# Kernel optimization log

Measured on AMD Instinct MI355X. Metric: run time of the kernel, lower is better.

Reference implementation:

```python
import jax, jax.numpy as jnp
import numpy as np

INPUT_SIZE = 512
OUTPUT_CLASS = 2
BATCH, INST_NUM = 4, 40000


def setup_inputs() -> dict:
    key = jax.random.key(0)
    ks = jax.random.split(key, 8)
    s_in = 1.0 / np.sqrt(INPUT_SIZE)
    s_h = 1.0 / np.sqrt(128)
    return {
        "feats": jax.random.normal(ks[0], (BATCH, INST_NUM, INPUT_SIZE), jnp.float32),
        "c": jax.random.normal(ks[1], (BATCH, INST_NUM, OUTPUT_CLASS), jnp.float32),
        "q_w1": jax.random.uniform(ks[2], (INPUT_SIZE, 128), jnp.float32, -s_in, s_in),
        "q_b1": jax.random.uniform(ks[3], (128,), jnp.float32, -s_in, s_in),
        "q_w2": jax.random.uniform(ks[4], (128, 128), jnp.float32, -s_h, s_h),
        "q_b2": jax.random.uniform(ks[5], (128,), jnp.float32, -s_h, s_h),
        "fcc_w": jax.random.uniform(ks[6], (OUTPUT_CLASS, OUTPUT_CLASS, INPUT_SIZE), jnp.float32, -s_in, s_in),
        "fcc_b": jax.random.uniform(ks[7], (OUTPUT_CLASS,), jnp.float32, -s_in, s_in),
    }


def _q_mlp(x, w1, b1, w2, b2):
    h = jax.nn.relu(x @ w1 + b1)
    return jnp.tanh(h @ w2 + b2)


def reference(feats, c, q_w1, q_b1, q_w2, q_b2, fcc_w, fcc_b):
    batch, inst_num, dim = feats.shape
    V = feats  # passing_v=False -> Identity
    Q = _q_mlp(feats, q_w1, q_b1, q_w2, q_b2)  # [b, n, 128]
    # top instance per class: sort descending, take first -> argmax along instances
    top_idx = jnp.argmax(c, axis=1)  # [b, output_class]
    m_feats = jnp.take_along_axis(feats, top_idx[:, :, None], axis=1)  # [b, oc, dim]
    q_max = _q_mlp(m_feats, q_w1, q_b1, q_w2, q_b2)  # [b, oc, 128]
    # NOTE: original divides by sqrt(Q.shape[1]) == sqrt(inst_num)
    scale = jnp.sqrt(jnp.float32(inst_num))
    A = jnp.einsum('bnk,bok->bno', Q, q_max) / scale  # [b, n, oc]
    A = jax.nn.softmax(A, axis=1)  # softmax over instances
    B = jnp.einsum('bno,bnd->bod', A, V)  # [b, oc, dim]
    # Conv1d(oc, oc, kernel=dim) on B -> full contraction over (in_ch, dim)
    C = jnp.einsum('bid,oid->bo', B, fcc_w) + fcc_b  # [b, oc]
    return C, A, B
```

## Files before the change

kernel.cpp:

```cpp
#include <hip/hip_runtime.h>
#include <hip/hip_bf16.h>

#define NB 4
#define NI 40000
#define DI 512
#define NH 128
#define TM 32
#define NT 1250

typedef __attribute__((ext_vector_type(8))) short bf16x8;
typedef __attribute__((ext_vector_type(4))) float f32x4;

__device__ __forceinline__ ushort f2b(float f) {
    union { float f; unsigned u; } x; x.f = f;
    unsigned r = x.u + 0x7FFFu + ((x.u >> 16) & 1u);
    return (ushort)(r >> 16);
}
__device__ __forceinline__ float b2f(ushort u) {
    union { unsigned u; float f; } x; x.u = ((unsigned)u) << 16;
    return x.f;
}

__global__ void k_wt(const float* __restrict__ w1, const float* __restrict__ w2,
                     ushort* __restrict__ w1t, ushort* __restrict__ w2t) {
    int idx = blockIdx.x * 256 + threadIdx.x;
    if (idx < 65536) {
        int j = idx >> 9, i = idx & 511;
        w1t[idx] = f2b(w1[i * 128 + j]);
    } else if (idx < 81920) {
        int r = idx - 65536;
        int j = r >> 7, k = r & 127;
        w2t[r] = f2b(w2[k * 128 + j]);
    }
}

__global__ void k_am1(const float* __restrict__ c, float* __restrict__ pv, int* __restrict__ pi) {
    int blk = blockIdx.x;
    int bo = blk >> 4, ch = blk & 15;
    int b = bo >> 1, o = bo & 1;
    __shared__ float rv[256];
    __shared__ int   ri[256];
    int tid = threadIdx.x;
    float bv = -3.402823466e38f; int bi = 0x7fffffff;
    for (int n = ch * 2500 + tid; n < (ch + 1) * 2500; n += 256) {
        float v = c[((size_t)b * NI + n) * 2 + o];
        if (v > bv || (v == bv && n < bi)) { bv = v; bi = n; }
    }
    rv[tid] = bv; ri[tid] = bi;
    __syncthreads();
    for (int s = 128; s > 0; s >>= 1) {
        if (tid < s) {
            if (rv[tid + s] > rv[tid] || (rv[tid + s] == rv[tid] && ri[tid + s] < ri[tid])) {
                rv[tid] = rv[tid + s]; ri[tid] = ri[tid + s];
            }
        }
        __syncthreads();
    }
    if (tid == 0) { pv[blk] = rv[0]; pi[blk] = ri[0]; }
}

__global__ void k_am2(const float* __restrict__ pv, const int* __restrict__ pi,
                      int* __restrict__ topidx) {
    int bo = blockIdx.x;
    if (threadIdx.x == 0) {
        float bv = -3.402823466e38f; int bi = 0x7fffffff;
        for (int ch = 0; ch < 16; ++ch) {
            float v = pv[bo * 16 + ch]; int idx = pi[bo * 16 + ch];
            if (v > bv || (v == bv && idx < bi)) { bv = v; bi = idx; }
        }
        topidx[bo] = bi;
    }
}

__global__ void k_qmax(const float* __restrict__ feats, const int* __restrict__ topidx,
                       const float* __restrict__ w1, const float* __restrict__ b1,
                       const float* __restrict__ w2, const float* __restrict__ b2,
                       float* __restrict__ qmax) {
    int bo = blockIdx.x;
    int b = bo >> 1;
    __shared__ float xs[DI];
    __shared__ float hs[NH];
    int tid = threadIdx.x;
    const float* x = feats + ((size_t)b * NI + topidx[bo]) * DI;
    if (tid < DI) xs[tid] = x[tid];
    __syncthreads();
    int j = tid >> 2, part = tid & 3;
    float p = 0.f;
    for (int i = part * 128; i < part * 128 + 128; ++i)
        p += xs[i] * w1[i * NH + j];
    p += __shfl_xor(p, 1); p += __shfl_xor(p, 2);
    if (part == 0) { float h = p + b1[j]; hs[j] = h > 0.f ? h : 0.f; }
    __syncthreads();
    p = 0.f;
    for (int i = part * 32; i < part * 32 + 32; ++i)
        p += hs[i] * w2[i * NH + j];
    p += __shfl_xor(p, 1); p += __shfl_xor(p, 2);
    if (part == 0) qmax[bo * NH + j] = tanhf(p + b2[j]);
}

__global__ __launch_bounds__(256, 3)
void k_main(const float* __restrict__ feats,
            const ushort* __restrict__ w1t, const ushort* __restrict__ w2t,
            const float* __restrict__ b1, const float* __restrict__ b2,
            const float* __restrict__ qmax,
            float* __restrict__ s_ws, float* __restrict__ zp, float* __restrict__ Up) {
    __shared__ ushort x_lds[TM * 512];
    __shared__ ushort h_lds[TM * 128];
    __shared__ float  sp_lds[4][TM][2];
    __shared__ float  e_lds[TM * 2];
    __shared__ float  qm_lds[2 * NH];

    const int tid = threadIdx.x;
    const int b = blockIdx.x / NT;
    const int t = blockIdx.x % NT;
    const int n0 = t * TM;

    qm_lds[tid] = qmax[b * 256 + tid];

    const float4* xg4 = (const float4*)(feats + ((size_t)(b * NI + n0)) * DI);
#pragma unroll
    for (int q = 0; q < 16; ++q) {
        int idx = tid + q * 256;
        int row = idx >> 7;
        int c4  = idx & 127;
        float4 v = xg4[idx];
        ushort4 u;
        u.x = f2b(v.x); u.y = f2b(v.y); u.z = f2b(v.z); u.w = f2b(v.w);
        int byteoff = (c4 * 8) ^ ((row & 7) << 4);
        *(ushort4*)((char*)x_lds + row * 1024 + byteoff) = u;
    }
    __syncthreads();

    const int wn = tid >> 6;
    const int lane = tid & 63;
    const int lr = lane & 15;
    const int lk = (lane >> 4) * 8;
    const int l4 = (lane >> 4) * 4;
    const int xsw = (lr & 7) << 4;

    const char* xrow0 = (const char*)x_lds + lr * 1024;
    const char* xrow1 = (const char*)x_lds + (16 + lr) * 1024;
    const ushort* w1b0 = w1t + (size_t)(wn * 32 + lr) * DI + lk;
    const ushort* w1b1 = w1t + (size_t)(wn * 32 + 16 + lr) * DI + lk;

    f32x4 acc[2][2] = {};
#pragma unroll 4
    for (int ks = 0; ks < 16; ++ks) {
        int kb = (ks * 32 + lk) * 2;
        bf16x8 a0 = *(const bf16x8*)(xrow0 + (kb ^ xsw));
        bf16x8 a1 = *(const bf16x8*)(xrow1 + (kb ^ xsw));
        bf16x8 b0 = *(const bf16x8*)(w1b0 + ks * 32);
        bf16x8 b1v = *(const bf16x8*)(w1b1 + ks * 32);
        acc[0][0] = __builtin_amdgcn_mfma_f32_16x16x32_bf16(a0, b0,  acc[0][0], 0, 0, 0);
        acc[0][1] = __builtin_amdgcn_mfma_f32_16x16x32_bf16(a0, b1v, acc[0][1], 0, 0, 0);
        acc[1][0] = __builtin_amdgcn_mfma_f32_16x16x32_bf16(a1, b0,  acc[1][0], 0, 0, 0);
        acc[1][1] = __builtin_amdgcn_mfma_f32_16x16x32_bf16(a1, b1v, acc[1][1], 0, 0, 0);
    }

#pragma unroll
    for (int m = 0; m < 2; ++m)
#pragma unroll
        for (int n = 0; n < 2; ++n) {
            int col = wn * 32 + n * 16 + lr;
            float bias = b1[col];
#pragma unroll
            for (int r = 0; r < 4; ++r) {
                int row = m * 16 + l4 + r;
                float v = acc[m][n][r] + bias;
                *(ushort*)((char*)h_lds + row * 256 + ((col * 2) ^ ((row & 7) << 4))) =
                    f2b(v > 0.f ? v : 0.f);
            }
        }
    __syncthreads();

    f32x4 acc2[2][2] = {};
#pragma unroll
    for (int ks = 0; ks < 4; ++ks) {
        int kb = (ks * 32 + lk) * 2;
        bf16x8 a0 = *(const bf16x8*)((const char*)h_lds + lr * 256 + (kb ^ xsw));
        bf16x8 a1 = *(const bf16x8*)((const char*)h_lds + (16 + lr) * 256 + (kb ^ xsw));
        bf16x8 b0 = *(const bf16x8*)(w2t + (wn * 32 + lr) * NH + ks * 32 + lk);
        bf16x8 b1v = *(const bf16x8*)(w2t + (wn * 32 + 16 + lr) * NH + ks * 32 + lk);
        acc2[0][0] = __builtin_amdgcn_mfma_f32_16x16x32_bf16(a0, b0,  acc2[0][0], 0, 0, 0);
        acc2[0][1] = __builtin_amdgcn_mfma_f32_16x16x32_bf16(a0, b1v, acc2[0][1], 0, 0, 0);
        acc2[1][0] = __builtin_amdgcn_mfma_f32_16x16x32_bf16(a1, b0,  acc2[1][0], 0, 0, 0);
        acc2[1][1] = __builtin_amdgcn_mfma_f32_16x16x32_bf16(a1, b1v, acc2[1][1], 0, 0, 0);
    }

#pragma unroll
    for (int m = 0; m < 2; ++m)
#pragma unroll
        for (int r = 0; r < 4; ++r) {
            float p0 = 0.f, p1 = 0.f;
#pragma unroll
            for (int n = 0; n < 2; ++n) {
                int col = wn * 32 + n * 16 + lr;
                float q = tanhf(acc2[m][n][r] + b2[col]);
                p0 += q * qm_lds[col];
                p1 += q * qm_lds[NH + col];
            }
            p0 += __shfl_xor(p0, 1); p1 += __shfl_xor(p1, 1);
            p0 += __shfl_xor(p0, 2); p1 += __shfl_xor(p1, 2);
            p0 += __shfl_xor(p0, 4); p1 += __shfl_xor(p1, 4);
            p0 += __shfl_xor(p0, 8); p1 += __shfl_xor(p1, 8);
            if (lr == 0) {
                int row = m * 16 + l4 + r;
                sp_lds[wn][row][0] = p0;
                sp_lds[wn][row][1] = p1;
            }
        }
    __syncthreads();

    if (tid < 64) {
        int row = tid >> 1, o = tid & 1;
        float s = (sp_lds[0][row][o] + sp_lds[1][row][o] +
                   sp_lds[2][row][o] + sp_lds[3][row][o]) * 0.005f;
        s_ws[((size_t)(b * NI + n0 + row)) * 2 + o] = s;
        float e = expf(s);
        e_lds[row * 2 + o] = e;
        float z = e;
        z += __shfl_xor(z, 2);  z += __shfl_xor(z, 4);
        z += __shfl_xor(z, 8);  z += __shfl_xor(z, 16);
        z += __shfl_xor(z, 32);
        if (tid < 2) zp[(b * NT + t) * 2 + tid] = z;
    }
    __syncthreads();

    {
        int bc = tid * 4;
        float u00 = 0.f, u01 = 0.f, u10 = 0.f, u11 = 0.f;
#pragma unroll 8
        for (int n = 0; n < TM; ++n) {
            unsigned v = *(const unsigned*)((const char*)x_lds + n * 1024 + (bc ^ ((n & 7) << 4)));
            float x0 = b2f((ushort)(v & 0xffff));
            float x1 = b2f((ushort)(v >> 16));
            float e0 = e_lds[n * 2], e1 = e_lds[n * 2 + 1];
            u00 += e0 * x0; u01 += e0 * x1;
            u10 += e1 * x0; u11 += e1 * x1;
        }
        size_t base = ((size_t)(b * NT + t) * 2) * DI;
        float2 v0; v0.x = u00; v0.y = u01;
        float2 v1; v1.x = u10; v1.y = u11;
        *(float2*)&Up[base + tid * 2] = v0;
        *(float2*)&Up[base + DI + tid * 2] = v1;
    }
}

__global__ void k_zred(const float* __restrict__ zp, float* __restrict__ Zt) {
    int bo = blockIdx.x; int b = bo >> 1, o = bo & 1;
    __shared__ float red[256];
    int tid = threadIdx.x;
    float z = 0.f;
    for (int t = tid; t < NT; t += 256) z += zp[(b * NT + t) * 2 + o];
    red[tid] = z; __syncthreads();
    for (int s = 128; s > 0; s >>= 1) {
        if (tid < s) red[tid] += red[tid + s];
        __syncthreads();
    }
    if (tid == 0) Zt[bo] = red[0];
}

__global__ void k_A(const float* __restrict__ s_ws, const float* __restrict__ Zt,
                    float* __restrict__ outA) {
    int idx = blockIdx.x * 256 + threadIdx.x;
    int b = idx / (NI * 2);
    int o = idx & 1;
    outA[idx] = expf(s_ws[idx]) / Zt[b * 2 + o];
}

__global__ void k_B1(const float* __restrict__ Up, float* __restrict__ Up2) {
    int blk = blockIdx.x;
    int bo = blk / 25, cch = blk % 25;
    int b = bo >> 1, o = bo & 1;
    int d = threadIdx.x;
    float u = 0.f;
    for (int t = cch * 50; t < cch * 50 + 50; ++t)
        u += Up[(((size_t)(b * NT + t)) * 2 + o) * DI + d];
    Up2[(size_t)blk * DI + d] = u;
}

__global__ void k_B2(const float* __restrict__ Up2, const float* __restrict__ Zt,
                     float* __restrict__ outB) {
    int bo = blockIdx.x; int d = threadIdx.x;
    float u = 0.f;
    for (int cc = 0; cc < 25; ++cc) u += Up2[(size_t)(bo * 25 + cc) * DI + d];
    outB[bo * DI + d] = u / Zt[bo];
}

__global__ void k_C(const float* __restrict__ outB, const float* __restrict__ fcc_w,
                    const float* __restrict__ fcc_b, float* __restrict__ outC) {
    int bo = blockIdx.x; int b = bo >> 1, o = bo & 1;
    __shared__ float red[256];
    int tid = threadIdx.x;
    float acc = 0.f;
    for (int idx = tid; idx < 2 * DI; idx += 256) {
        int i = idx >> 9, d = idx & 511;
        acc += outB[(b * 2 + i) * DI + d] * fcc_w[o * (2 * DI) + i * DI + d];
    }
    red[tid] = acc; __syncthreads();
    for (int s = 128; s > 0; s >>= 1) {
        if (tid < s) red[tid] += red[tid + s];
        __syncthreads();
    }
    if (tid == 0) outC[bo] = red[0] + fcc_b[o];
}

extern "C" void kernel_launch(void* const* d_in, const int* in_sizes, int n_in,
                              void* d_out, int out_size, void* d_ws, size_t ws_size,
                              hipStream_t stream) {
    const float* feats = (const float*)d_in[0];
    const float* c     = (const float*)d_in[1];
    const float* q_w1  = (const float*)d_in[2];
    const float* q_b1  = (const float*)d_in[3];
    const float* q_w2  = (const float*)d_in[4];
    const float* q_b2  = (const float*)d_in[5];
    const float* fcc_w = (const float*)d_in[6];
    const float* fcc_b = (const float*)d_in[7];
    float* out = (float*)d_out;

    char* w = (char*)d_ws;
    ushort* w1t  = (ushort*)(w);
    ushort* w2t  = (ushort*)(w + 131072);
    float* qmaxb = (float*)(w + 163840);
    int*   topi  = (int*)(w + 167936);
    float* Zt    = (float*)(w + 167968);
    float* pv    = (float*)(w + 168000);
    int*   pi    = (int*)(w + 168512);
    float* s_ws  = (float*)(w + 169024);
    float* zp    = (float*)(w + 1449024);
    float* Up2   = (float*)(w + 1489024);
    float* Up    = (float*)(w + 1898624);

    float* outC = out;
    float* outA = out + 8;
    float* outB = out + 8 + NB * NI * 2;

    k_wt<<<320, 256, 0, stream>>>(q_w1, q_w2, w1t, w2t);
    k_am1<<<128, 256, 0, stream>>>(c, pv, pi);
    k_am2<<<8, 64, 0, stream>>>(pv, pi, topi);
    k_qmax<<<8, 512, 0, stream>>>(feats, topi, q_w1, q_b1, q_w2, q_b2, qmaxb);
    k_main<<<NB * NT, 256, 0, stream>>>(feats, w1t, w2t, q_b1, q_b2, qmaxb, s_ws, zp, Up);
    k_zred<<<8, 256, 0, stream>>>(zp, Zt);
    k_A<<<NB * NI * 2 / 256, 256, 0, stream>>>(s_ws, Zt, outA);
    k_B1<<<200, 512, 0, stream>>>(Up, Up2);
    k_B2<<<8, 512, 0, stream>>>(Up2, Zt, outB);
    k_C<<<8, 256, 0, stream>>>(outB, fcc_w, fcc_b, outC);
}
```

Baseline: 204.4 us.

## Restructure main kernel to per-wave 16-row tiles with direct global loads

The main kernel now gives each wave 16 rows of instances and all 128 hidden columns, reading feats straight from global into MFMA operands and dropping the shared x tile and most block barriers. It also stores exp scores so k_A skips the exp, swaps tanhf for a fast exp-based tanh, folds the argmax final step into k_qmax, and merges the two B reduction kernels into one. The aim is less LDS traffic, fewer syncs and fewer launches. In exchange feats is read twice from global (MLP and weighted sum), each lane loads the full w1 and w2 from global, and unnormalised exps are stored without max subtraction.

```diff
diff --git a/kernel.cpp b/kernel.cpp
--- a/kernel.cpp
+++ b/kernel.cpp
@@ -5,8 +5,6 @@
 #define NI 40000
 #define DI 512
 #define NH 128
-#define TM 32
-#define NT 1250
 
 typedef __attribute__((ext_vector_type(8))) short bf16x8;
 typedef __attribute__((ext_vector_type(4))) float f32x4;
@@ -16,9 +14,10 @@
     unsigned r = x.u + 0x7FFFu + ((x.u >> 16) & 1u);
     return (ushort)(r >> 16);
 }
-__device__ __forceinline__ float b2f(ushort u) {
-    union { unsigned u; float f; } x; x.u = ((unsigned)u) << 16;
-    return x.f;
+__device__ __forceinline__ float tanh_fast(float x) {
+    x = fminf(15.f, fmaxf(-15.f, x));
+    float e = __expf(2.f * x);
+    return (e - 1.f) / (e + 1.f);
 }
 
 __global__ void k_wt(const float* __restrict__ w1, const float* __restrict__ w2,
@@ -59,20 +58,8 @@
     if (tid == 0) { pv[blk] = rv[0]; pi[blk] = ri[0]; }
 }
 
-__global__ void k_am2(const float* __restrict__ pv, const int* __restrict__ pi,
-                      int* __restrict__ topidx) {
-    int bo = blockIdx.x;
-    if (threadIdx.x == 0) {
-        float bv = -3.402823466e38f; int bi = 0x7fffffff;
-        for (int ch = 0; ch < 16; ++ch) {
-            float v = pv[bo * 16 + ch]; int idx = pi[bo * 16 + ch];
-            if (v > bv || (v == bv && idx < bi)) { bv = v; bi = idx; }
-        }
-        topidx[bo] = bi;
-    }
-}
-
-__global__ void k_qmax(const float* __restrict__ feats, const int* __restrict__ topidx,
+__global__ void k_qmax(const float* __restrict__ feats,
+                       const float* __restrict__ pv, const int* __restrict__ pi,
                        const float* __restrict__ w1, const float* __restrict__ b1,
                        const float* __restrict__ w2, const float* __restrict__ b2,
                        float* __restrict__ qmax) {
@@ -80,8 +67,18 @@
     int b = bo >> 1;
     __shared__ float xs[DI];
     __shared__ float hs[NH];
+    __shared__ int s_idx;
     int tid = threadIdx.x;
-    const float* x = feats + ((size_t)b * NI + topidx[bo]) * DI;
+    if (tid == 0) {
+        float bv = -3.402823466e38f; int bi = 0x7fffffff;
+        for (int ch = 0; ch < 16; ++ch) {
+            float v = pv[bo * 16 + ch]; int idx = pi[bo * 16 + ch];
+            if (v > bv || (v == bv && idx < bi)) { bv = v; bi = idx; }
+        }
+        s_idx = bi;
+    }
+    __syncthreads();
+    const float* x = feats + ((size_t)b * NI + s_idx) * DI;
     if (tid < DI) xs[tid] = x[tid];
     __syncthreads();
     int j = tid >> 2, part = tid & 3;
@@ -99,150 +96,159 @@
 }
 
 __global__ __launch_bounds__(256, 3)
-void k_main(const float* __restrict__ feats,
-            const ushort* __restrict__ w1t, const ushort* __restrict__ w2t,
-            const float* __restrict__ b1, const float* __restrict__ b2,
-            const float* __restrict__ qmax,
-            float* __restrict__ s_ws, float* __restrict__ zp, float* __restrict__ Up) {
-    __shared__ ushort x_lds[TM * 512];
-    __shared__ ushort h_lds[TM * 128];
-    __shared__ float  sp_lds[4][TM][2];
-    __shared__ float  e_lds[TM * 2];
-    __shared__ float  qm_lds[2 * NH];
-
-    const int tid = threadIdx.x;
-    const int b = blockIdx.x / NT;
-    const int t = blockIdx.x % NT;
-    const int n0 = t * TM;
-
-    qm_lds[tid] = qmax[b * 256 + tid];
-
-    const float4* xg4 = (const float4*)(feats + ((size_t)(b * NI + n0)) * DI);
-#pragma unroll
-    for (int q = 0; q < 16; ++q) {
-        int idx = tid + q * 256;
-        int row = idx >> 7;
-        int c4  = idx & 127;
-        float4 v = xg4[idx];
-        ushort4 u;
-        u.x = f2b(v.x); u.y = f2b(v.y); u.z = f2b(v.z); u.w = f2b(v.w);
-        int byteoff = (c4 * 8) ^ ((row & 7) << 4);
-        *(ushort4*)((char*)x_lds + row * 1024 + byteoff) = u;
-    }
-    __syncthreads();
-
-    const int wn = tid >> 6;
+void k_mlp(const float* __restrict__ feats,
+           const ushort* __restrict__ w1t, const ushort* __restrict__ w2t,
+           const float* __restrict__ b1, const float* __restrict__ b2,
+           const float* __restrict__ qmax,
+           float* __restrict__ ews, float* __restrict__ zp, float* __restrict__ Up) {
+    __shared__ ushort h_lds[4][2048];
+    __shared__ float  u_lds[4][2][DI];
+
+    const int tid  = threadIdx.x;
+    const int wv   = tid >> 6;
     const int lane = tid & 63;
-    const int lr = lane & 15;
-    const int lk = (lane >> 4) * 8;
-    const int l4 = (lane >> 4) * 4;
-    const int xsw = (lr & 7) << 4;
-
-    const char* xrow0 = (const char*)x_lds + lr * 1024;
-    const char* xrow1 = (const char*)x_lds + (16 + lr) * 1024;
-    const ushort* w1b0 = w1t + (size_t)(wn * 32 + lr) * DI + lk;
-    const ushort* w1b1 = w1t + (size_t)(wn * 32 + 16 + lr) * DI + lk;
-
-    f32x4 acc[2][2] = {};
-#pragma unroll 4
-    for (int ks = 0; ks < 16; ++ks) {
-        int kb = (ks * 32 + lk) * 2;
-        bf16x8 a0 = *(const bf16x8*)(xrow0 + (kb ^ xsw));
-        bf16x8 a1 = *(const bf16x8*)(xrow1 + (kb ^ xsw));
-        bf16x8 b0 = *(const bf16x8*)(w1b0 + ks * 32);
-        bf16x8 b1v = *(const bf16x8*)(w1b1 + ks * 32);
-        acc[0][0] = __builtin_amdgcn_mfma_f32_16x16x32_bf16(a0, b0,  acc[0][0], 0, 0, 0);
-        acc[0][1] = __builtin_amdgcn_mfma_f32_16x16x32_bf16(a0, b1v, acc[0][1], 0, 0, 0);
-        acc[1][0] = __builtin_amdgcn_mfma_f32_16x16x32_bf16(a1, b0,  acc[1][0], 0, 0, 0);
-        acc[1][1] = __builtin_amdgcn_mfma_f32_16x16x32_bf16(a1, b1v, acc[1][1], 0, 0, 0);
-    }
-
-#pragma unroll
-    for (int m = 0; m < 2; ++m)
-#pragma unroll
-        for (int n = 0; n < 2; ++n) {
-            int col = wn * 32 + n * 16 + lr;
-            float bias = b1[col];
+    const int lr   = lane & 15;
+    const int lkg  = lane >> 4;
+    const int lk   = lkg * 8;
+    const int l4   = lkg * 4;
+
+    const int bk  = blockIdx.x;
+    const int b   = bk / 625;
+    const int blk = bk - b * 625;
+    const int n0  = blk * 64 + wv * 16;
+    const float* fb = feats + ((size_t)b * NI + n0) * DI;
+
+    float qm0[8], qm1[8], b1v[8], b2v[8];
+#pragma unroll
+    for (int n = 0; n < 8; ++n) {
+        int col = n * 16 + lr;
+        qm0[n] = qmax[b * 256 + col];
+        qm1[n] = qmax[b * 256 + NH + col];
+        b1v[n] = b1[col];
+        b2v[n] = b2[col];
+    }
+
+    f32x4 acc[8] = {};
+    {
+        const float* arow = fb + (size_t)lr * DI + lk;
+#pragma unroll
+        for (int kc = 0; kc < 16; ++kc) {
+            float4 xa = *(const float4*)(arow + kc * 32);
+            float4 xb = *(const float4*)(arow + kc * 32 + 4);
+            unsigned p0, p1, p2, p3;
+            asm("v_cvt_pk_bf16_f32 %0, %1, %2" : "=v"(p0) : "v"(xa.x), "v"(xa.y));
+            asm("v_cvt_pk_bf16_f32 %0, %1, %2" : "=v"(p1) : "v"(xa.z), "v"(xa.w));
+            asm("v_cvt_pk_bf16_f32 %0, %1, %2" : "=v"(p2) : "v"(xb.x), "v"(xb.y));
+            asm("v_cvt_pk_bf16_f32 %0, %1, %2" : "=v"(p3) : "v"(xb.z), "v"(xb.w));
+            union { unsigned u[4]; bf16x8 v; } A;
+            A.u[0] = p0; A.u[1] = p1; A.u[2] = p2; A.u[3] = p3;
+#pragma unroll
+            for (int n = 0; n < 8; ++n) {
+                bf16x8 w = *(const bf16x8*)&w1t[(size_t)(n * 16 + lr) * DI + kc * 32 + lk];
+                acc[n] = __builtin_amdgcn_mfma_f32_16x16x32_bf16(A.v, w, acc[n], 0, 0, 0);
+            }
+        }
+    }
+
+    {
+        char* hb = (char*)&h_lds[wv][0];
+#pragma unroll
+        for (int n = 0; n < 8; ++n) {
+            int col2 = (n * 16 + lr) * 2;
 #pragma unroll
             for (int r = 0; r < 4; ++r) {
-                int row = m * 16 + l4 + r;
-                float v = acc[m][n][r] + bias;
-                *(ushort*)((char*)h_lds + row * 256 + ((col * 2) ^ ((row & 7) << 4))) =
+                int row = l4 + r;
+                float v = acc[n][r] + b1v[n];
+                *(ushort*)(hb + row * 256 + (col2 ^ ((row & 7) << 4))) =
                     f2b(v > 0.f ? v : 0.f);
             }
         }
-    __syncthreads();
-
-    f32x4 acc2[2][2] = {};
-#pragma unroll
-    for (int ks = 0; ks < 4; ++ks) {
-        int kb = (ks * 32 + lk) * 2;
-        bf16x8 a0 = *(const bf16x8*)((const char*)h_lds + lr * 256 + (kb ^ xsw));
-        bf16x8 a1 = *(const bf16x8*)((const char*)h_lds + (16 + lr) * 256 + (kb ^ xsw));
-        bf16x8 b0 = *(const bf16x8*)(w2t + (wn * 32 + lr) * NH + ks * 32 + lk);
-        bf16x8 b1v = *(const bf16x8*)(w2t + (wn * 32 + 16 + lr) * NH + ks * 32 + lk);
-        acc2[0][0] = __builtin_amdgcn_mfma_f32_16x16x32_bf16(a0, b0,  acc2[0][0], 0, 0, 0);
-        acc2[0][1] = __builtin_amdgcn_mfma_f32_16x16x32_bf16(a0, b1v, acc2[0][1], 0, 0, 0);
-        acc2[1][0] = __builtin_amdgcn_mfma_f32_16x16x32_bf16(a1, b0,  acc2[1][0], 0, 0, 0);
-        acc2[1][1] = __builtin_amdgcn_mfma_f32_16x16x32_bf16(a1, b1v, acc2[1][1], 0, 0, 0);
-    }
-
-#pragma unroll
-    for (int m = 0; m < 2; ++m)
+    }
+
+    f32x4 q[8] = {};
+    {
+        const char* hr = (const char*)&h_lds[wv][0] + lr * 256;
+        const int rsw = (lr & 7) << 4;
+#pragma unroll
+        for (int kc = 0; kc < 4; ++kc) {
+            bf16x8 a = *(const bf16x8*)(hr + ((kc * 64 + lk * 2) ^ rsw));
+#pragma unroll
+            for (int n = 0; n < 8; ++n) {
+                bf16x8 w = *(const bf16x8*)&w2t[(size_t)(n * 16 + lr) * NH + kc * 32 + lk];
+                q[n] = __builtin_amdgcn_mfma_f32_16x16x32_bf16(a, w, q[n], 0, 0, 0);
+            }
+        }
+    }
+
+    float e0[4], e1[4];
+    {
+        float p0[4] = {}, p1[4] = {};
+#pragma unroll
+        for (int n = 0; n < 8; ++n)
+#pragma unroll
+            for (int r = 0; r < 4; ++r) {
+                float qq = tanh_fast(q[n][r] + b2v[n]);
+                p0[r] += qq * qm0[n];
+                p1[r] += qq * qm1[n];
+            }
 #pragma unroll
         for (int r = 0; r < 4; ++r) {
-            float p0 = 0.f, p1 = 0.f;
-#pragma unroll
-            for (int n = 0; n < 2; ++n) {
-                int col = wn * 32 + n * 16 + lr;
-                float q = tanhf(acc2[m][n][r] + b2[col]);
-                p0 += q * qm_lds[col];
-                p1 += q * qm_lds[NH + col];
-            }
-            p0 += __shfl_xor(p0, 1); p1 += __shfl_xor(p1, 1);
-            p0 += __shfl_xor(p0, 2); p1 += __shfl_xor(p1, 2);
-            p0 += __shfl_xor(p0, 4); p1 += __shfl_xor(p1, 4);
-            p0 += __shfl_xor(p0, 8); p1 += __shfl_xor(p1, 8);
-            if (lr == 0) {
-                int row = m * 16 + l4 + r;
-                sp_lds[wn][row][0] = p0;
-                sp_lds[wn][row][1] = p1;
-            }
-        }
-    __syncthreads();
-
-    if (tid < 64) {
-        int row = tid >> 1, o = tid & 1;
-        float s = (sp_lds[0][row][o] + sp_lds[1][row][o] +
-                   sp_lds[2][row][o] + sp_lds[3][row][o]) * 0.005f;
-        s_ws[((size_t)(b * NI + n0 + row)) * 2 + o] = s;
-        float e = expf(s);
-        e_lds[row * 2 + o] = e;
-        float z = e;
-        z += __shfl_xor(z, 2);  z += __shfl_xor(z, 4);
-        z += __shfl_xor(z, 8);  z += __shfl_xor(z, 16);
-        z += __shfl_xor(z, 32);
-        if (tid < 2) zp[(b * NT + t) * 2 + tid] = z;
-    }
-    __syncthreads();
-
-    {
-        int bc = tid * 4;
-        float u00 = 0.f, u01 = 0.f, u10 = 0.f, u11 = 0.f;
-#pragma unroll 8
-        for (int n = 0; n < TM; ++n) {
-            unsigned v = *(const unsigned*)((const char*)x_lds + n * 1024 + (bc ^ ((n & 7) << 4)));
-            float x0 = b2f((ushort)(v & 0xffff));
-            float x1 = b2f((ushort)(v >> 16));
-            float e0 = e_lds[n * 2], e1 = e_lds[n * 2 + 1];
-            u00 += e0 * x0; u01 += e0 * x1;
-            u10 += e1 * x0; u11 += e1 * x1;
-        }
-        size_t base = ((size_t)(b * NT + t) * 2) * DI;
-        float2 v0; v0.x = u00; v0.y = u01;
-        float2 v1; v1.x = u10; v1.y = u11;
-        *(float2*)&Up[base + tid * 2] = v0;
-        *(float2*)&Up[base + DI + tid * 2] = v1;
+            p0[r] += __shfl_xor(p0[r], 1); p1[r] += __shfl_xor(p1[r], 1);
+            p0[r] += __shfl_xor(p0[r], 2); p1[r] += __shfl_xor(p1[r], 2);
+            p0[r] += __shfl_xor(p0[r], 4); p1[r] += __shfl_xor(p1[r], 4);
+            p0[r] += __shfl_xor(p0[r], 8); p1[r] += __shfl_xor(p1[r], 8);
+            e0[r] = __expf(p0[r] * 0.005f);
+            e1[r] = __expf(p1[r] * 0.005f);
+        }
+    }
+
+    if (lr == 0) {
+        size_t base = ((size_t)b * NI + n0 + l4) * 2;
+#pragma unroll
+        for (int r = 0; r < 4; ++r) {
+            ews[base + r * 2]     = e0[r];
+            ews[base + r * 2 + 1] = e1[r];
+        }
+    }
+    {
+        float z0 = e0[0] + e0[1] + e0[2] + e0[3];
+        float z1 = e1[0] + e1[1] + e1[2] + e1[3];
+        z0 += __shfl_xor(z0, 16); z1 += __shfl_xor(z1, 16);
+        z0 += __shfl_xor(z0, 32); z1 += __shfl_xor(z1, 32);
+        if (lane == 0) {
+            int t = blk * 4 + wv;
+            zp[(b * 2500 + t) * 2]     = z0;
+            zp[(b * 2500 + t) * 2 + 1] = z1;
+        }
+    }
+
+    float4 u00 = {0,0,0,0}, u01 = {0,0,0,0}, u10 = {0,0,0,0}, u11 = {0,0,0,0};
+#pragma unroll
+    for (int r = 0; r < 16; ++r) {
+        float4 xA = *(const float4*)(fb + (size_t)r * DI + lane * 4);
+        float4 xB = *(const float4*)(fb + (size_t)r * DI + 256 + lane * 4);
+        float er0 = __shfl(e0[r & 3], (r >> 2) * 16 + (lane & 15));
+        float er1 = __shfl(e1[r & 3], (r >> 2) * 16 + (lane & 15));
+        u00.x += er0 * xA.x; u00.y += er0 * xA.y; u00.z += er0 * xA.z; u00.w += er0 * xA.w;
+        u01.x += er0 * xB.x; u01.y += er0 * xB.y; u01.z += er0 * xB.z; u01.w += er0 * xB.w;
+        u10.x += er1 * xA.x; u10.y += er1 * xA.y; u10.z += er1 * xA.z; u10.w += er1 * xA.w;
+        u11.x += er1 * xB.x; u11.y += er1 * xB.y; u11.z += er1 * xB.z; u11.w += er1 * xB.w;
+    }
+
+    *(float4*)&u_lds[wv][0][lane * 4]       = u00;
+    *(float4*)&u_lds[wv][0][256 + lane * 4] = u01;
+    *(float4*)&u_lds[wv][1][lane * 4]       = u10;
+    *(float4*)&u_lds[wv][1][256 + lane * 4] = u11;
+    __syncthreads();
+    {
+        int o = tid >> 7, d4 = tid & 127;
+        float4 s = {0,0,0,0};
+#pragma unroll
+        for (int w = 0; w < 4; ++w) {
+            float4 v = *(const float4*)&u_lds[w][o][d4 * 4];
+            s.x += v.x; s.y += v.y; s.z += v.z; s.w += v.w;
+        }
+        *(float4*)&Up[(((size_t)(b * 625 + blk)) * 2 + o) * DI + d4 * 4] = s;
     }
 }
 
@@ -251,7 +257,7 @@
     __shared__ float red[256];
     int tid = threadIdx.x;
     float z = 0.f;
-    for (int t = tid; t < NT; t += 256) z += zp[(b * NT + t) * 2 + o];
+    for (int t = tid; t < 2500; t += 256) z += zp[(b * 2500 + t) * 2 + o];
     red[tid] = z; __syncthreads();
     for (int s = 128; s > 0; s >>= 1) {
         if (tid < s) red[tid] += red[tid + s];
@@ -260,31 +266,29 @@
     if (tid == 0) Zt[bo] = red[0];
 }
 
-__global__ void k_A(const float* __restrict__ s_ws, const float* __restrict__ Zt,
+__global__ void k_A(const float* __restrict__ ews, const float* __restrict__ Zt,
                     float* __restrict__ outA) {
     int idx = blockIdx.x * 256 + threadIdx.x;
     int b = idx / (NI * 2);
     int o = idx & 1;
-    outA[idx] = expf(s_ws[idx]) / Zt[b * 2 + o];
-}
-
-__global__ void k_B1(const float* __restrict__ Up, float* __restrict__ Up2) {
-    int blk = blockIdx.x;
-    int bo = blk / 25, cch = blk % 25;
-    int b = bo >> 1, o = bo & 1;
-    int d = threadIdx.x;
+    outA[idx] = ews[idx] / Zt[b * 2 + o];
+}
+
+__global__ void k_B(const float* __restrict__ Up, const float* __restrict__ Zt,
+                    float* __restrict__ outB) {
+    __shared__ float r_lds[4][64];
+    const int bo = blockIdx.x >> 3, ch = blockIdx.x & 7;
+    const int b = bo >> 1, o = bo & 1;
+    const int tid = threadIdx.x;
+    const int pg = tid >> 6, dl = tid & 63;
+    const int d = ch * 64 + dl;
     float u = 0.f;
-    for (int t = cch * 50; t < cch * 50 + 50; ++t)
-        u += Up[(((size_t)(b * NT + t)) * 2 + o) * DI + d];
-    Up2[(size_t)blk * DI + d] = u;
-}
-
-__global__ void k_B2(const float* __restrict__ Up2, const float* __restrict__ Zt,
-                     float* __restrict__ outB) {
-    int bo = blockIdx.x; int d = threadIdx.x;
-    float u = 0.f;
-    for (int cc = 0; cc < 25; ++cc) u += Up2[(size_t)(bo * 25 + cc) * DI + d];
-    outB[bo * DI + d] = u / Zt[bo];
+    for (int j = pg; j < 625; j += 4)
+        u += Up[((size_t)(b * 625 + j) * 2 + o) * DI + d];
+    r_lds[pg][dl] = u;
+    __syncthreads();
+    if (tid < 64)
+        outB[bo * DI + d] = (r_lds[0][dl] + r_lds[1][dl] + r_lds[2][dl] + r_lds[3][dl]) / Zt[bo];
 }
 
 __global__ void k_C(const float* __restrict__ outB, const float* __restrict__ fcc_w,
@@ -322,14 +326,12 @@
     ushort* w1t  = (ushort*)(w);
     ushort* w2t  = (ushort*)(w + 131072);
     float* qmaxb = (float*)(w + 163840);
-    int*   topi  = (int*)(w + 167936);
-    float* Zt    = (float*)(w + 167968);
-    float* pv    = (float*)(w + 168000);
-    int*   pi    = (int*)(w + 168512);
-    float* s_ws  = (float*)(w + 169024);
+    float* Zt    = (float*)(w + 167936);
+    float* pv    = (float*)(w + 167968);
+    int*   pi    = (int*)(w + 168480);
+    float* ews   = (float*)(w + 169024);
     float* zp    = (float*)(w + 1449024);
-    float* Up2   = (float*)(w + 1489024);
-    float* Up    = (float*)(w + 1898624);
+    float* Up    = (float*)(w + 1529088);
 
     float* outC = out;
     float* outA = out + 8;
@@ -337,12 +339,10 @@
 
     k_wt<<<320, 256, 0, stream>>>(q_w1, q_w2, w1t, w2t);
     k_am1<<<128, 256, 0, stream>>>(c, pv, pi);
-    k_am2<<<8, 64, 0, stream>>>(pv, pi, topi);
-    k_qmax<<<8, 512, 0, stream>>>(feats, topi, q_w1, q_b1, q_w2, q_b2, qmaxb);
-    k_main<<<NB * NT, 256, 0, stream>>>(feats, w1t, w2t, q_b1, q_b2, qmaxb, s_ws, zp, Up);
+    k_qmax<<<8, 512, 0, stream>>>(feats, pv, pi, q_w1, q_b1, q_w2, q_b2, qmaxb);
+    k_mlp<<<2500, 256, 0, stream>>>(feats, w1t, w2t, q_b1, q_b2, qmaxb, ews, zp, Up);
     k_zred<<<8, 256, 0, stream>>>(zp, Zt);
-    k_A<<<NB * NI * 2 / 256, 256, 0, stream>>>(s_ws, Zt, outA);
-    k_B1<<<200, 512, 0, stream>>>(Up, Up2);
-    k_B2<<<8, 512, 0, stream>>>(Up2, Zt, outB);
+    k_A<<<NB * NI * 2 / 256, 256, 0, stream>>>(ews, Zt, outA);
+    k_B<<<64, 256, 0, stream>>>(Up, Zt, outB);
     k_C<<<8, 256, 0, stream>>>(outB, fcc_w, fcc_b, outC);
 }
```

After: 339.0 us. +65.9%, slower.
